# Kernel optimization log

Hardware: AMD Instinct MI355X
Metric: run time of the kernel (lower is better)

Reference implementation:

```python
import jax, jax.numpy as jnp
import numpy as np

S, H, I, E, K = 16384, 1024, 512, 64, 2
CAP = 640  # capacity per expert: ceil(S*K/E * 1.25)


def setup_inputs() -> dict:
    key = jax.random.key(0)
    k0, k1, k2, k3, k4 = jax.random.split(key, 5)
    x = jax.random.normal(k0, (S, H), jnp.float32)
    w_gate = jax.random.normal(k1, (H, E), jnp.float32) * 0.02
    wg = jax.random.normal(k2, (E, H, I), jnp.float32) * 0.02
    wu = jax.random.normal(k3, (E, H, I), jnp.float32) * 0.02
    wd = jax.random.normal(k4, (E, I, H), jnp.float32) * 0.02
    return {"x": x, "w_gate": w_gate, "wg": wg, "wu": wu, "wd": wd}


def reference(x, w_gate, wg, wu, wd):
    # --- gate (fp32) + softmax ---
    logits = x.astype(jnp.float32) @ w_gate                      # [S,E]
    prob = jax.nn.softmax(logits, axis=-1)
    topk_p, topk_e = jax.lax.top_k(prob, K)                      # [S,K]

    # --- capacity-based dispatch (token-major, route-minor order, as in torch loop) ---
    flat_e = topk_e.reshape(-1)                                  # [S*K]
    onehot = jax.nn.one_hot(flat_e, E, dtype=jnp.int32)          # [S*K,E]
    pos = jnp.cumsum(onehot, axis=0)[jnp.arange(S * K), flat_e] - 1  # slot within expert
    valid = pos < CAP                                            # [S*K]

    combine_w = jnp.where(valid.reshape(S, K), topk_p, 0.0)      # dropped -> 0 weight
    slot_idx = jnp.where(valid, flat_e * CAP + pos, E * CAP)     # dummy row for drops
    x_rep = jnp.repeat(x, K, axis=0)                             # [S*K,H], row i = x[i//K]
    y = jnp.zeros((E * CAP + 1, H), x.dtype).at[slot_idx].set(x_rep)[: E * CAP]
    dispatched = y.reshape(E, CAP, H)

    # --- per-expert SwiGLU MLP (grouped GEMMs) ---
    g = jnp.einsum("ech,ehi->eci", dispatched, wg)
    u = jnp.einsum("ech,ehi->eci", dispatched, wu)
    expert_out = jnp.einsum("eci,eih->ech", jax.nn.silu(g) * u, wd)  # [E,CAP,H]

    # --- normalize weights and combine (gather + weighted sum) ---
    cw = combine_w / jnp.clip(combine_w.sum(-1, keepdims=True), 1e-12, None)
    scatter_index = jnp.where(valid, flat_e * CAP + pos, -1).reshape(S, K)
    gathered = expert_out.reshape(E * CAP, H)[scatter_index]     # [S,K,H]; -1 wraps, weight=0
    out = jnp.einsum("sk,skh->sh", cw, gathered)                 # [S,H]

    router_loss = jnp.zeros((1,), jnp.float32)
    return out, cw, router_loss, logits
```

## Files before the change

### kernel.cpp

```cpp
#include <hip/hip_runtime.h>
#include <hip/hip_bf16.h>

constexpr int S_TOK = 16384;
constexpr int HDIM  = 1024;
constexpr int IDIM  = 512;
constexpr int NEXP  = 64;
constexpr int CAPC  = 640;
constexpr int NCHUNK = 128;

typedef __attribute__((ext_vector_type(8))) short bf16x8;
typedef __attribute__((ext_vector_type(4))) short short4v;
typedef __attribute__((ext_vector_type(4))) float f32x4;

__device__ __forceinline__ float bf2f(unsigned short u){
  return __uint_as_float(((unsigned)u) << 16);
}
__device__ __forceinline__ unsigned short f2bf(float f){
  unsigned u = __float_as_uint(f);
  return (unsigned short)((u + 0x7fffu + ((u >> 16) & 1u)) >> 16);
}
__device__ __forceinline__ unsigned pk2cvt(float a, float b){
  unsigned r;
  asm volatile("v_cvt_pk_bf16_f32 %0, %1, %2" : "=v"(r) : "v"(a), "v"(b));
  return r;
}
__device__ __forceinline__ void gload_lds16(const void* g, void* l){
  __builtin_amdgcn_global_load_lds((const __attribute__((address_space(1))) unsigned*)g,
                                   (__attribute__((address_space(3))) unsigned*)l, 16, 0, 0);
}
__device__ __forceinline__ unsigned ldsoff(const void* p){ return (unsigned)(size_t)p; }
__device__ __forceinline__ void trread2(unsigned addr, short4v& lo, short4v& hi){
  asm volatile("ds_read_b64_tr_b16 %0, %2\n\t"
               "ds_read_b64_tr_b16 %1, %2 offset:512"
               : "=&v"(lo), "=&v"(hi) : "v"(addr));
}

__global__ __launch_bounds__(256) void gate_kernel(
    const float* __restrict__ x, const float* __restrict__ wgate,
    float* __restrict__ logits_out, float* __restrict__ topk_p,
    int* __restrict__ flat_e, float* __restrict__ rl_out)
{
  __shared__ float xs[4][HDIM];
  const int w = threadIdx.x >> 6, lane = threadIdx.x & 63;
  const int tok = blockIdx.x * 4 + w;
  const float4* xr = (const float4*)(x + (size_t)tok * HDIM);
  float4* xd = (float4*)(&xs[w][0]);
#pragma unroll
  for (int j = 0; j < 4; ++j) xd[j * 64 + lane] = xr[j * 64 + lane];
  __syncthreads();
  float acc = 0.f;
#pragma unroll 8
  for (int h = 0; h < HDIM; ++h)
    acc = fmaf(xs[w][h], wgate[h * NEXP + lane], acc);
  logits_out[(size_t)tok * NEXP + lane] = acc;
  float m = acc;
#pragma unroll
  for (int d = 1; d < 64; d <<= 1) m = fmaxf(m, __shfl_xor(m, d));
  float p = expf(acc - m);
  float sum = p;
#pragma unroll
  for (int d = 1; d < 64; d <<= 1) sum += __shfl_xor(sum, d);
  float prob = p / sum;
  float v = prob; int idx = lane;
#pragma unroll
  for (int d = 1; d < 64; d <<= 1){
    float ov = __shfl_xor(v, d); int oi = __shfl_xor(idx, d);
    if (ov > v || (ov == v && oi < idx)){ v = ov; idx = oi; }
  }
  const int e1 = idx; const float p1 = v;
  v = (lane == e1) ? -1.f : prob; idx = lane;
#pragma unroll
  for (int d = 1; d < 64; d <<= 1){
    float ov = __shfl_xor(v, d); int oi = __shfl_xor(idx, d);
    if (ov > v || (ov == v && oi < idx)){ v = ov; idx = oi; }
  }
  if (lane == 0){
    flat_e[tok * 2]     = e1;  flat_e[tok * 2 + 1] = idx;
    topk_p[tok * 2]     = p1;  topk_p[tok * 2 + 1] = v;
  }
  if (tok == 0 && lane == 0) rl_out[0] = 0.f;
}

__global__ __launch_bounds__(256) void hist_kernel(const int* __restrict__ flat_e,
                                                   int* __restrict__ counts)
{
  __shared__ int hh[NEXP];
  const int t = threadIdx.x;
  if (t < NEXP) hh[t] = 0;
  __syncthreads();
  const int e = flat_e[blockIdx.x * 256 + t];
  atomicAdd(&hh[e], 1);
  __syncthreads();
  if (t < NEXP) counts[blockIdx.x * NEXP + t] = hh[t];
}

__global__ __launch_bounds__(256) void offsets_kernel(const int* __restrict__ counts,
                                                      int* __restrict__ offs,
                                                      int* __restrict__ etot)
{
  const int w = threadIdx.x >> 6, lane = threadIdx.x & 63;
  const int e = blockIdx.x * 4 + w;
  int v0 = counts[lane * NEXP + e];
  int v1 = counts[(64 + lane) * NEXP + e];
  int s0 = v0, s1 = v1;
#pragma unroll
  for (int d = 1; d < 64; d <<= 1){
    int n0 = __shfl_up(s0, d); if (lane >= d) s0 += n0;
    int n1 = __shfl_up(s1, d); if (lane >= d) s1 += n1;
  }
  const int tot0 = __shfl(s0, 63);
  offs[lane * NEXP + e]        = s0 - v0;
  offs[(64 + lane) * NEXP + e] = tot0 + s1 - v1;
  if (lane == 63) etot[e] = tot0 + s1;
}

__global__ __launch_bounds__(256) void place_kernel(
    const int* __restrict__ flat_e, const float* __restrict__ topk_p,
    const int* __restrict__ offs, int* __restrict__ entry_slot,
    int* __restrict__ token_of_slot, float* __restrict__ cw_out)
{
  __shared__ int es[256];
  __shared__ float wsh[256];
  const int t = threadIdx.x;
  const int i = blockIdx.x * 256 + t;
  const int e = flat_e[i];
  es[t] = e;
  __syncthreads();
  int local = 0;
  for (int j = 0; j < t; ++j) local += (es[j] == e);
  const int pos = offs[blockIdx.x * NEXP + e] + local;
  const bool valid = pos < CAPC;
  const int slot = e * CAPC + pos;
  entry_slot[i] = valid ? slot : -1;
  if (valid) token_of_slot[slot] = i >> 1;
  const float p = topk_p[i];
  wsh[t] = valid ? p : 0.f;
  __syncthreads();
  const float wme = wsh[t], wo = wsh[t ^ 1];
  cw_out[i] = wme / fmaxf(wme + wo, 1e-12f);
}

__global__ __launch_bounds__(256) void adisp_kernel(
    const float* __restrict__ x, const int* __restrict__ token_of_slot,
    const int* __restrict__ etot, unsigned short* __restrict__ adisp)
{
  const int slot = blockIdx.x;
  const int e = slot / CAPC, c = slot - e * CAPC;
  int cnt = etot[e]; if (cnt > CAPC) cnt = CAPC;
  if (c >= cnt) return;
  const int tok = token_of_slot[slot];
  const int t = threadIdx.x;
  float4 v = ((const float4*)(x + (size_t)tok * HDIM))[t];
  ushort4 o; o.x = f2bf(v.x); o.y = f2bf(v.y); o.z = f2bf(v.z); o.w = f2bf(v.w);
  ((ushort4*)(adisp + (size_t)slot * HDIM))[t] = o;
}


__global__ __launch_bounds__(512, 2) void gemm1_kernel(
    const unsigned short* __restrict__ adisp,
    const float* __restrict__ wg, const float* __restrict__ wu,
    const int* __restrict__ etot,
    unsigned short* __restrict__ hbuf)
{
  constexpr int NK1 = HDIM / 32;
  __shared__ unsigned short As[3][128 * 32];
  __shared__ unsigned short Bs[3][2 * 128 * 32];
  const int bb = blockIdx.x;
  const int lb = (bb & 7) * 160 + (bb >> 3);
  const int e = lb / 20; const int r2 = lb - e * 20;
  const int nt = r2 / 5, mt = r2 - nt * 5;
  { int cnt = etot[e]; if (cnt > CAPC) cnt = CAPC;
    if (mt * 128 >= cnt) return; }
  const int t = threadIdx.x, w = t >> 6, lane = t & 63;
  const int wr = w >> 2, wc = w & 3;
  const size_t arow0 = (size_t)e * CAPC + (size_t)mt * 128;
  const unsigned short* abase = adisp + arow0 * HDIM;
  const float* gsrc = wg + (size_t)e * HDIM * IDIM + nt * 128;
  const float* usrc = wu + (size_t)e * HDIM * IDIM + nt * 128;

  int aoff; { int row = t >> 2, jsrc = (t & 3) ^ ((row >> 1) & 3);
              aoff = row * HDIM + jsrc * 8; }
  const int g_ = w >> 1, par = w & 1;
  const int dk = (lane >> 1) & 3, h8 = lane & 1, ng = lane >> 3;
  const int bk = 8 * g_ + 4 * par + dk;
  const int bn0 = ng * 16 + h8 * 8;
  const int bgo = bk * IDIM + bn0;
  const unsigned bwo = (unsigned)((((ng * 2 + par) * 4 + g_) * 64) + dk * 16 + h8 * 8);

  f32x4 ag[4][2], au[4][2];
#pragma unroll
  for (int i = 0; i < 4; ++i)
#pragma unroll
    for (int j = 0; j < 2; ++j)
#pragma unroll
      for (int q = 0; q < 4; ++q){ ag[i][j][q] = 0.f; au[i][j][q] = 0.f; }

  float4 g0a, g0b, u0a, u0b, g1a, g1b, u1a, u1b;

#define G1_LOAD(KB, RA, RB, RC, RD) {                                          \
    const float* gp_ = gsrc + (size_t)(KB) * IDIM + bgo;                       \
    const float* up_ = usrc + (size_t)(KB) * IDIM + bgo;                       \
    RA = *(const float4*)gp_;       RB = *(const float4*)(gp_ + 4);            \
    RC = *(const float4*)up_;       RD = *(const float4*)(up_ + 4); }

#define G1_STORE(NB, WA, WB, WC, WD) {                                         \
    *(uint4*)&Bs[NB][bwo] = make_uint4(pk2cvt(WA.x,WA.y), pk2cvt(WA.z,WA.w),   \
                                       pk2cvt(WB.x,WB.y), pk2cvt(WB.z,WB.w));  \
    *(uint4*)&Bs[NB][4096 + bwo] = make_uint4(pk2cvt(WC.x,WC.y), pk2cvt(WC.z,WC.w), \
                                       pk2cvt(WD.x,WD.y), pk2cvt(WD.z,WD.w)); }

#define G1_STEP(TI, LA, LB, LC, LD, WA, WB, WC, WD) {                          \
    const int cur_ = (TI) % 3;                                                 \
    const bool pf_ = (TI) + 2 < NK1;                                           \
    if (pf_){                                                                  \
      const int kb2_ = ((TI) + 2) * 32;                                        \
      gload_lds16(abase + aoff + kb2_, &As[((TI) + 2) % 3][w * 64 * 8]);       \
      G1_LOAD(kb2_, LA, LB, LC, LD);                                           \
    }                                                                          \
    { const int j8_ = lane >> 4;                                               \
      bf16x8 af_[4], bg_[2], bu_[2];                                           \
      _Pragma("unroll")                                                        \
      for (int m = 0; m < 4; ++m){                                             \
        int row_ = wr * 64 + m * 16 + (lane & 15);                             \
        af_[m] = *(const bf16x8*)&As[cur_][row_ * 32 + ((j8_ ^ ((row_ >> 1) & 3)) * 8)]; \
      }                                                                        \
      const unsigned b0_ = ldsoff(&Bs[cur_][0]);                               \
      _Pragma("unroll")                                                        \
      for (int n = 0; n < 2; ++n){                                             \
        unsigned ao_ = (unsigned)((wc * 2 + n) * 1024 + lane * 8);             \
        short4v l0_, l1_, m0_, m1_;                                            \
        trread2(b0_ + ao_, l0_, l1_);                                          \
        bg_[n] = __builtin_shufflevector(l0_, l1_, 0,1,2,3,4,5,6,7);           \
        trread2(b0_ + 8192 + ao_, m0_, m1_);                                   \
        bu_[n] = __builtin_shufflevector(m0_, m1_, 0,1,2,3,4,5,6,7);           \
      }                                                                        \
      asm volatile("s_waitcnt lgkmcnt(0)" ::: "memory");                       \
      __builtin_amdgcn_sched_barrier(0);                                       \
      __builtin_amdgcn_s_setprio(1);                                           \
      _Pragma("unroll")                                                        \
      for (int m = 0; m < 4; ++m)                                              \
        _Pragma("unroll")                                                      \
        for (int n = 0; n < 2; ++n){                                           \
          ag[m][n] = __builtin_amdgcn_mfma_f32_16x16x32_bf16(af_[m], bg_[n], ag[m][n], 0, 0, 0); \
          au[m][n] = __builtin_amdgcn_mfma_f32_16x16x32_bf16(af_[m], bu_[n], au[m][n], 0, 0, 0); \
        }                                                                      \
      __builtin_amdgcn_s_setprio(0);                                           \
    }                                                                          \
    if ((TI) + 1 < NK1){                                                       \
      if (pf_) asm volatile("s_waitcnt vmcnt(5)" ::: "memory");                \
      else     asm volatile("s_waitcnt vmcnt(0)" ::: "memory");                \
      G1_STORE(((TI) + 1) % 3, WA, WB, WC, WD);                                \
    }                                                                          \
    asm volatile("s_waitcnt lgkmcnt(0)" ::: "memory");                         \
    __builtin_amdgcn_s_barrier();                                              \
    __builtin_amdgcn_sched_barrier(0);                                         \
  }

  gload_lds16(abase + aoff + 0,  &As[0][w * 64 * 8]);
  G1_LOAD(0,  g0a, g0b, u0a, u0b);
  gload_lds16(abase + aoff + 32, &As[1][w * 64 * 8]);
  G1_LOAD(32, g1a, g1b, u1a, u1b);
  asm volatile("s_waitcnt vmcnt(5)" ::: "memory");
  G1_STORE(0, g0a, g0b, u0a, u0b);
  asm volatile("s_waitcnt lgkmcnt(0)" ::: "memory");
  __builtin_amdgcn_s_barrier();

  for (int tb = 0; tb < NK1; tb += 2){
    G1_STEP(tb,     g0a, g0b, u0a, u0b,  g1a, g1b, u1a, u1b);
    G1_STEP(tb + 1, g1a, g1b, u1a, u1b,  g0a, g0b, u0a, u0b);
  }
#undef G1_STEP
#undef G1_STORE
#undef G1_LOAD

#pragma unroll
  for (int m = 0; m < 4; ++m)
#pragma unroll
    for (int n = 0; n < 2; ++n)
#pragma unroll
      for (int q = 0; q < 4; ++q){
        int row = wr * 64 + m * 16 + (lane >> 4) * 4 + q;
        int col = nt * 128 + wc * 32 + n * 16 + (lane & 15);
        float gv = ag[m][n][q], uv = au[m][n][q];
        float hv = gv / (1.f + expf(-gv)) * uv;
        hbuf[(arow0 + row) * IDIM + col] = f2bf(hv);
      }
}

__global__ __launch_bounds__(512, 2) void gemm2_kernel(
    const unsigned short* __restrict__ hbuf,
    const float* __restrict__ wd,
    const int* __restrict__ etot,
    unsigned short* __restrict__ eo)
{
  constexpr int NK2 = IDIM / 32;
  __shared__ unsigned short As[3][128 * 32];
  __shared__ unsigned short Bs[3][2 * 128 * 32];
  const int bb = blockIdx.x;
  const int lb = (bb & 7) * 160 + (bb >> 3);
  const int e = lb / 20; const int r2 = lb - e * 20;
  const int nt = r2 / 5, mt = r2 - nt * 5;
  { int cnt = etot[e]; if (cnt > CAPC) cnt = CAPC;
    if (mt * 128 >= cnt) return; }
  const int t = threadIdx.x, w = t >> 6, lane = t & 63;
  const int wr = w >> 2, wc = w & 3;
  const size_t arow0 = (size_t)e * CAPC + (size_t)mt * 128;
  const unsigned short* abase = hbuf + arow0 * IDIM;
  const float* dsrc = wd + (size_t)e * IDIM * HDIM + nt * 256;

  int aoff; { int row = t >> 2, jsrc = (t & 3) ^ ((row >> 1) & 3);
              aoff = row * IDIM + jsrc * 8; }
  const int g_ = w >> 1, par = w & 1;
  const int dk = (lane >> 1) & 3, h8 = lane & 1, ng = lane >> 3;
  const int bk = 8 * g_ + 4 * par + dk;
  const int bn0 = ng * 16 + h8 * 8;
  const int bgo = bk * HDIM + bn0;
  const unsigned bwo = (unsigned)((((ng * 2 + par) * 4 + g_) * 64) + dk * 16 + h8 * 8);

  f32x4 ac[4][4];
#pragma unroll
  for (int i = 0; i < 4; ++i)
#pragma unroll
    for (int j = 0; j < 4; ++j)
#pragma unroll
      for (int q = 0; q < 4; ++q) ac[i][j][q] = 0.f;

  float4 p0a, p0b, p1a, p1b, q0a, q0b, q1a, q1b;

#define G2_LOAD(KB, RA, RB, RC, RD) {                                          \
    const float* gp_ = dsrc + (size_t)(KB) * HDIM + bgo;                       \
    RA = *(const float4*)gp_;         RB = *(const float4*)(gp_ + 4);          \
    RC = *(const float4*)(gp_ + 128); RD = *(const float4*)(gp_ + 132); }

#define G2_STORE(NB, WA, WB, WC, WD) {                                         \
    *(uint4*)&Bs[NB][bwo] = make_uint4(pk2cvt(WA.x,WA.y), pk2cvt(WA.z,WA.w),   \
                                       pk2cvt(WB.x,WB.y), pk2cvt(WB.z,WB.w));  \
    *(uint4*)&Bs[NB][4096 + bwo] = make_uint4(pk2cvt(WC.x,WC.y), pk2cvt(WC.z,WC.w), \
                                       pk2cvt(WD.x,WD.y), pk2cvt(WD.z,WD.w)); }

#define G2_STEP(TI, LA, LB, LC, LD, WA, WB, WC, WD) {                          \
    const int cur_ = (TI) % 3;                                                 \
    const bool pf_ = (TI) + 2 < NK2;                                           \
    if (pf_){                                                                  \
      const int kb2_ = ((TI) + 2) * 32;                                        \
      gload_lds16(abase + aoff + kb2_, &As[((TI) + 2) % 3][w * 64 * 8]);       \
      G2_LOAD(kb2_, LA, LB, LC, LD);                                           \
    }                                                                          \
    { const int j8_ = lane >> 4;                                               \
      bf16x8 af_[4], bf_[4];                                                   \
      _Pragma("unroll")                                                        \
      for (int m = 0; m < 4; ++m){                                             \
        int row_ = wr * 64 + m * 16 + (lane & 15);                             \
        af_[m] = *(const bf16x8*)&As[cur_][row_ * 32 + ((j8_ ^ ((row_ >> 1) & 3)) * 8)]; \
      }                                                                        \
      const unsigned b0_ = ldsoff(&Bs[cur_][0]) + (unsigned)(wc >> 1) * 8192;  \
      _Pragma("unroll")                                                        \
      for (int n = 0; n < 4; ++n){                                             \
        unsigned ao_ = (unsigned)(((wc & 1) * 4 + n) * 1024 + lane * 8);       \
        short4v l0_, l1_;                                                      \
        trread2(b0_ + ao_, l0_, l1_);                                          \
        bf_[n] = __builtin_shufflevector(l0_, l1_, 0,1,2,3,4,5,6,7);           \
      }                                                                        \
      asm volatile("s_waitcnt lgkmcnt(0)" ::: "memory");                       \
      __builtin_amdgcn_sched_barrier(0);                                       \
      __builtin_amdgcn_s_setprio(1);                                           \
      _Pragma("unroll")                                                        \
      for (int m = 0; m < 4; ++m)                                              \
        _Pragma("unroll")                                                      \
        for (int n = 0; n < 4; ++n)                                            \
          ac[m][n] = __builtin_amdgcn_mfma_f32_16x16x32_bf16(af_[m], bf_[n], ac[m][n], 0, 0, 0); \
      __builtin_amdgcn_s_setprio(0);                                           \
    }                                                                          \
    if ((TI) + 1 < NK2){                                                       \
      if (pf_) asm volatile("s_waitcnt vmcnt(5)" ::: "memory");                \
      else     asm volatile("s_waitcnt vmcnt(0)" ::: "memory");                \
      G2_STORE(((TI) + 1) % 3, WA, WB, WC, WD);                                \
    }                                                                          \
    asm volatile("s_waitcnt lgkmcnt(0)" ::: "memory");                         \
    __builtin_amdgcn_s_barrier();                                              \
    __builtin_amdgcn_sched_barrier(0);                                         \
  }

  gload_lds16(abase + aoff + 0,  &As[0][w * 64 * 8]);
  G2_LOAD(0,  p0a, p0b, q0a, q0b);
  gload_lds16(abase + aoff + 32, &As[1][w * 64 * 8]);
  G2_LOAD(32, p1a, p1b, q1a, q1b);
  asm volatile("s_waitcnt vmcnt(5)" ::: "memory");
  G2_STORE(0, p0a, p0b, q0a, q0b);
  asm volatile("s_waitcnt lgkmcnt(0)" ::: "memory");
  __builtin_amdgcn_s_barrier();

  for (int tb = 0; tb < NK2; tb += 2){
    G2_STEP(tb,     p0a, p0b, q0a, q0b,  p1a, p1b, q1a, q1b);
    G2_STEP(tb + 1, p1a, p1b, q1a, q1b,  p0a, p0b, q0a, q0b);
  }
#undef G2_STEP
#undef G2_STORE
#undef G2_LOAD

#pragma unroll
  for (int m = 0; m < 4; ++m)
#pragma unroll
    for (int n = 0; n < 4; ++n)
#pragma unroll
      for (int q = 0; q < 4; ++q){
        int row = wr * 64 + m * 16 + (lane >> 4) * 4 + q;
        int col = nt * 256 + wc * 64 + n * 16 + (lane & 15);
        eo[(arow0 + row) * HDIM + col] = f2bf(ac[m][n][q]);
      }
}

__global__ __launch_bounds__(256) void combine_kernel(
    const unsigned short* __restrict__ eo, const int* __restrict__ entry_slot,
    const float* __restrict__ cw, float* __restrict__ out)
{
  const int s = blockIdx.x, t = threadIdx.x;
  const int s0 = entry_slot[2 * s], s1 = entry_slot[2 * s + 1];
  const float w0 = cw[2 * s], w1 = cw[2 * s + 1];
  const int c = t * 4;
  float r0 = 0.f, r1 = 0.f, r2 = 0.f, r3 = 0.f;
  if (s0 >= 0){
    ushort4 vq = *(const ushort4*)&eo[(size_t)s0 * HDIM + c];
    r0 += w0 * bf2f(vq.x); r1 += w0 * bf2f(vq.y); r2 += w0 * bf2f(vq.z); r3 += w0 * bf2f(vq.w);
  }
  if (s1 >= 0){
    ushort4 vq = *(const ushort4*)&eo[(size_t)s1 * HDIM + c];
    r0 += w1 * bf2f(vq.x); r1 += w1 * bf2f(vq.y); r2 += w1 * bf2f(vq.z); r3 += w1 * bf2f(vq.w);
  }
  ((float4*)(out + (size_t)s * HDIM))[t] = make_float4(r0, r1, r2, r3);
}

extern "C" void kernel_launch(void* const* d_in, const int* in_sizes, int n_in,
                              void* d_out, int out_size, void* d_ws, size_t ws_size,
                              hipStream_t stream) {
  (void)in_sizes; (void)n_in; (void)out_size; (void)ws_size;
  const float* x     = (const float*)d_in[0];
  const float* wgate = (const float*)d_in[1];
  const float* wg    = (const float*)d_in[2];
  const float* wu    = (const float*)d_in[3];
  const float* wd    = (const float*)d_in[4];

  float* out        = (float*)d_out;
  float* cw_out     = out + (size_t)S_TOK * HDIM;
  float* rl_out     = cw_out + (size_t)S_TOK * 2;
  float* logits_out = rl_out + 1;

  char* w8 = (char*)d_ws;
  size_t off = 0;
  auto alloc = [&](size_t bytes){ size_t r = off; off += (bytes + 255) & ~(size_t)255; return r; };
  int*   flat_e_ws        = (int*)  (w8 + alloc((size_t)32768 * 4));
  float* topk_p_ws        = (float*)(w8 + alloc((size_t)32768 * 4));
  int*   counts_ws        = (int*)  (w8 + alloc((size_t)NCHUNK * NEXP * 4));
  int*   offs_ws          = (int*)  (w8 + alloc((size_t)NCHUNK * NEXP * 4));
  int*   etot_ws          = (int*)  (w8 + alloc((size_t)NEXP * 4));
  int*   entry_slot_ws    = (int*)  (w8 + alloc((size_t)32768 * 4));
  int*   token_of_slot_ws = (int*)  (w8 + alloc((size_t)NEXP * CAPC * 4));
  unsigned short* hbuf_ws = (unsigned short*)(w8 + alloc((size_t)NEXP * CAPC * IDIM * 2));
  unsigned short* adisp_ws= (unsigned short*)(w8 + alloc((size_t)NEXP * CAPC * HDIM * 2));
  unsigned short* eo_ws   = adisp_ws;

  gate_kernel   <<<S_TOK / 4, 256, 0, stream>>>(x, wgate, logits_out, topk_p_ws, flat_e_ws, rl_out);
  hist_kernel   <<<NCHUNK,    256, 0, stream>>>(flat_e_ws, counts_ws);
  offsets_kernel<<<16,        256, 0, stream>>>(counts_ws, offs_ws, etot_ws);
  place_kernel  <<<NCHUNK,    256, 0, stream>>>(flat_e_ws, topk_p_ws, offs_ws,
                                                entry_slot_ws, token_of_slot_ws, cw_out);
  adisp_kernel  <<<NEXP * CAPC, 256, 0, stream>>>(x, token_of_slot_ws, etot_ws, adisp_ws);
  gemm1_kernel  <<<NEXP * 20, 512, 0, stream>>>(adisp_ws, wg, wu, etot_ws, hbuf_ws);
  gemm2_kernel  <<<NEXP * 20, 512, 0, stream>>>(hbuf_ws, wd, etot_ws, eo_ws);
  combine_kernel<<<S_TOK,     256, 0, stream>>>(eo_ws, entry_slot_ws, cw_out, out);
}
```

Baseline: 538.2 us.

## Switch grouped GEMMs to 32x32x16 MFMA with re-laid-out B tiles in LDS

Replaces the 16x16x32 bf16 MFMA tiling in both expert GEMM kernels with 32x32x16 MFMA instructions. The B-operand LDS layout, the transposed-read offsets and the epilogue row/column mapping are reworked to match the larger instruction shape. The aim is fewer MFMA and LDS read instructions per k-step and better operand reuse per instruction. The risks are different LDS bank-conflict patterns and accumulator register pressure from the 16-wide fragments.

```diff
diff --git a/kernel.cpp b/kernel.cpp
--- a/kernel.cpp
+++ b/kernel.cpp
@@ -10,7 +10,7 @@
 
 typedef __attribute__((ext_vector_type(8))) short bf16x8;
 typedef __attribute__((ext_vector_type(4))) short short4v;
-typedef __attribute__((ext_vector_type(4))) float f32x4;
+typedef __attribute__((ext_vector_type(16))) float f32x16;
 
 __device__ __forceinline__ float bf2f(unsigned short u){
   return __uint_as_float(((unsigned)u) << 16);
@@ -31,7 +31,7 @@
 __device__ __forceinline__ unsigned ldsoff(const void* p){ return (unsigned)(size_t)p; }
 __device__ __forceinline__ void trread2(unsigned addr, short4v& lo, short4v& hi){
   asm volatile("ds_read_b64_tr_b16 %0, %2\n\t"
-               "ds_read_b64_tr_b16 %1, %2 offset:512"
+               "ds_read_b64_tr_b16 %1, %2 offset:128"
                : "=&v"(lo), "=&v"(hi) : "v"(addr));
 }
 
@@ -180,20 +180,20 @@
 
   int aoff; { int row = t >> 2, jsrc = (t & 3) ^ ((row >> 1) & 3);
               aoff = row * HDIM + jsrc * 8; }
-  const int g_ = w >> 1, par = w & 1;
-  const int dk = (lane >> 1) & 3, h8 = lane & 1, ng = lane >> 3;
-  const int bk = 8 * g_ + 4 * par + dk;
-  const int bn0 = ng * 16 + h8 * 8;
+  const int ks_ = w >> 2, khalf = (w >> 1) & 1, par = w & 1;
+  const int dk = (lane >> 1) & 3, h8 = lane & 1;
+  const int n16 = (lane >> 3) & 1, n32 = lane >> 4;
+  const int bk = 16 * ks_ + 8 * khalf + 4 * par + dk;
+  const int bn0 = n32 * 32 + n16 * 16 + h8 * 8;
   const int bgo = bk * IDIM + bn0;
-  const unsigned bwo = (unsigned)((((ng * 2 + par) * 4 + g_) * 64) + dk * 16 + h8 * 8);
-
-  f32x4 ag[4][2], au[4][2];
-#pragma unroll
-  for (int i = 0; i < 4; ++i)
-#pragma unroll
-    for (int j = 0; j < 2; ++j)
-#pragma unroll
-      for (int q = 0; q < 4; ++q){ ag[i][j][q] = 0.f; au[i][j][q] = 0.f; }
+  const unsigned bwo = (unsigned)(n32 * 1024 + ks_ * 512 + (khalf * 2 + n16) * 128
+                                  + par * 64 + dk * 16 + h8 * 8);
+
+  f32x16 ag[2], au[2];
+#pragma unroll
+  for (int i = 0; i < 2; ++i)
+#pragma unroll
+    for (int q = 0; q < 16; ++q){ ag[i][q] = 0.f; au[i][q] = 0.f; }
 
   float4 g0a, g0b, u0a, u0b, g1a, g1b, u1a, u1b;
 
@@ -217,33 +217,28 @@
       gload_lds16(abase + aoff + kb2_, &As[((TI) + 2) % 3][w * 64 * 8]);       \
       G1_LOAD(kb2_, LA, LB, LC, LD);                                           \
     }                                                                          \
-    { const int j8_ = lane >> 4;                                               \
-      bf16x8 af_[4], bg_[2], bu_[2];                                           \
-      _Pragma("unroll")                                                        \
-      for (int m = 0; m < 4; ++m){                                             \
-        int row_ = wr * 64 + m * 16 + (lane & 15);                             \
-        af_[m] = *(const bf16x8*)&As[cur_][row_ * 32 + ((j8_ ^ ((row_ >> 1) & 3)) * 8)]; \
-      }                                                                        \
-      const unsigned b0_ = ldsoff(&Bs[cur_][0]);                               \
-      _Pragma("unroll")                                                        \
-      for (int n = 0; n < 2; ++n){                                             \
-        unsigned ao_ = (unsigned)((wc * 2 + n) * 1024 + lane * 8);             \
-        short4v l0_, l1_, m0_, m1_;                                            \
-        trread2(b0_ + ao_, l0_, l1_);                                          \
-        bg_[n] = __builtin_shufflevector(l0_, l1_, 0,1,2,3,4,5,6,7);           \
-        trread2(b0_ + 8192 + ao_, m0_, m1_);                                   \
-        bu_[n] = __builtin_shufflevector(m0_, m1_, 0,1,2,3,4,5,6,7);           \
-      }                                                                        \
+    const unsigned b0_ = ldsoff(&Bs[cur_][0]) + (unsigned)wc * 2048            \
+                         + (unsigned)(lane >> 4) * 256 + (unsigned)(lane & 15) * 8; \
+    _Pragma("unroll")                                                          \
+    for (int ksi = 0; ksi < 2; ++ksi){                                         \
+      bf16x8 af0_, af1_, bg_, bu_;                                             \
+      { int row0_ = wr * 64 + (lane & 31);                                     \
+        int row1_ = row0_ + 32;                                                \
+        int koct_ = ksi * 2 + (lane >> 5);                                     \
+        af0_ = *(const bf16x8*)&As[cur_][row0_ * 32 + ((koct_ ^ ((row0_ >> 1) & 3)) * 8)]; \
+        af1_ = *(const bf16x8*)&As[cur_][row1_ * 32 + ((koct_ ^ ((row1_ >> 1) & 3)) * 8)]; } \
+      { short4v l0_, l1_, m0_, m1_;                                            \
+        trread2(b0_ + (unsigned)ksi * 1024, l0_, l1_);                         \
+        bg_ = __builtin_shufflevector(l0_, l1_, 0,1,2,3,4,5,6,7);              \
+        trread2(b0_ + 8192 + (unsigned)ksi * 1024, m0_, m1_);                  \
+        bu_ = __builtin_shufflevector(m0_, m1_, 0,1,2,3,4,5,6,7); }            \
       asm volatile("s_waitcnt lgkmcnt(0)" ::: "memory");                       \
       __builtin_amdgcn_sched_barrier(0);                                       \
       __builtin_amdgcn_s_setprio(1);                                           \
-      _Pragma("unroll")                                                        \
-      for (int m = 0; m < 4; ++m)                                              \
-        _Pragma("unroll")                                                      \
-        for (int n = 0; n < 2; ++n){                                           \
-          ag[m][n] = __builtin_amdgcn_mfma_f32_16x16x32_bf16(af_[m], bg_[n], ag[m][n], 0, 0, 0); \
-          au[m][n] = __builtin_amdgcn_mfma_f32_16x16x32_bf16(af_[m], bu_[n], au[m][n], 0, 0, 0); \
-        }                                                                      \
+      ag[0] = __builtin_amdgcn_mfma_f32_32x32x16_bf16(af0_, bg_, ag[0], 0, 0, 0); \
+      au[0] = __builtin_amdgcn_mfma_f32_32x32x16_bf16(af0_, bu_, au[0], 0, 0, 0); \
+      ag[1] = __builtin_amdgcn_mfma_f32_32x32x16_bf16(af1_, bg_, ag[1], 0, 0, 0); \
+      au[1] = __builtin_amdgcn_mfma_f32_32x32x16_bf16(af1_, bu_, au[1], 0, 0, 0); \
       __builtin_amdgcn_s_setprio(0);                                           \
     }                                                                          \
     if ((TI) + 1 < NK1){                                                       \
@@ -274,17 +269,15 @@
 #undef G1_LOAD
 
 #pragma unroll
-  for (int m = 0; m < 4; ++m)
-#pragma unroll
-    for (int n = 0; n < 2; ++n)
-#pragma unroll
-      for (int q = 0; q < 4; ++q){
-        int row = wr * 64 + m * 16 + (lane >> 4) * 4 + q;
-        int col = nt * 128 + wc * 32 + n * 16 + (lane & 15);
-        float gv = ag[m][n][q], uv = au[m][n][q];
-        float hv = gv / (1.f + expf(-gv)) * uv;
-        hbuf[(arow0 + row) * IDIM + col] = f2bf(hv);
-      }
+  for (int mp = 0; mp < 2; ++mp)
+#pragma unroll
+    for (int r = 0; r < 16; ++r){
+      int row = wr * 64 + mp * 32 + (r & 3) + 8 * (r >> 2) + 4 * (lane >> 5);
+      int col = nt * 128 + wc * 32 + (lane & 31);
+      float gv = ag[mp][r], uv = au[mp][r];
+      float hv = gv / (1.f + expf(-gv)) * uv;
+      hbuf[(arow0 + row) * IDIM + col] = f2bf(hv);
+    }
 }
 
 __global__ __launch_bounds__(512, 2) void gemm2_kernel(
@@ -310,20 +303,22 @@
 
   int aoff; { int row = t >> 2, jsrc = (t & 3) ^ ((row >> 1) & 3);
               aoff = row * IDIM + jsrc * 8; }
-  const int g_ = w >> 1, par = w & 1;
-  const int dk = (lane >> 1) & 3, h8 = lane & 1, ng = lane >> 3;
-  const int bk = 8 * g_ + 4 * par + dk;
-  const int bn0 = ng * 16 + h8 * 8;
+  const int ks_ = w >> 2, khalf = (w >> 1) & 1, par = w & 1;
+  const int dk = (lane >> 1) & 3, h8 = lane & 1;
+  const int n16 = (lane >> 3) & 1, n32 = lane >> 4;
+  const int bk = 16 * ks_ + 8 * khalf + 4 * par + dk;
+  const int bn0 = n32 * 32 + n16 * 16 + h8 * 8;
   const int bgo = bk * HDIM + bn0;
-  const unsigned bwo = (unsigned)((((ng * 2 + par) * 4 + g_) * 64) + dk * 16 + h8 * 8);
-
-  f32x4 ac[4][4];
-#pragma unroll
-  for (int i = 0; i < 4; ++i)
-#pragma unroll
-    for (int j = 0; j < 4; ++j)
-#pragma unroll
-      for (int q = 0; q < 4; ++q) ac[i][j][q] = 0.f;
+  const unsigned bwo = (unsigned)(n32 * 1024 + ks_ * 512 + (khalf * 2 + n16) * 128
+                                  + par * 64 + dk * 16 + h8 * 8);
+
+  f32x16 ac[2][2];
+#pragma unroll
+  for (int i = 0; i < 2; ++i)
+#pragma unroll
+    for (int j = 0; j < 2; ++j)
+#pragma unroll
+      for (int q = 0; q < 16; ++q) ac[i][j][q] = 0.f;
 
   float4 p0a, p0b, p1a, p1b, q0a, q0b, q1a, q1b;
 
@@ -346,29 +341,28 @@
       gload_lds16(abase + aoff + kb2_, &As[((TI) + 2) % 3][w * 64 * 8]);       \
       G2_LOAD(kb2_, LA, LB, LC, LD);                                           \
     }                                                                          \
-    { const int j8_ = lane >> 4;                                               \
-      bf16x8 af_[4], bf_[4];                                                   \
-      _Pragma("unroll")                                                        \
-      for (int m = 0; m < 4; ++m){                                             \
-        int row_ = wr * 64 + m * 16 + (lane & 15);                             \
-        af_[m] = *(const bf16x8*)&As[cur_][row_ * 32 + ((j8_ ^ ((row_ >> 1) & 3)) * 8)]; \
-      }                                                                        \
-      const unsigned b0_ = ldsoff(&Bs[cur_][0]) + (unsigned)(wc >> 1) * 8192;  \
-      _Pragma("unroll")                                                        \
-      for (int n = 0; n < 4; ++n){                                             \
-        unsigned ao_ = (unsigned)(((wc & 1) * 4 + n) * 1024 + lane * 8);       \
-        short4v l0_, l1_;                                                      \
-        trread2(b0_ + ao_, l0_, l1_);                                          \
-        bf_[n] = __builtin_shufflevector(l0_, l1_, 0,1,2,3,4,5,6,7);           \
-      }                                                                        \
+    const unsigned b0_ = ldsoff(&Bs[cur_][0]) + (unsigned)wc * 4096            \
+                         + (unsigned)(lane >> 4) * 256 + (unsigned)(lane & 15) * 8; \
+    _Pragma("unroll")                                                          \
+    for (int ksi = 0; ksi < 2; ++ksi){                                         \
+      bf16x8 af0_, af1_, b0f_, b1f_;                                           \
+      { int row0_ = wr * 64 + (lane & 31);                                     \
+        int row1_ = row0_ + 32;                                                \
+        int koct_ = ksi * 2 + (lane >> 5);                                     \
+        af0_ = *(const bf16x8*)&As[cur_][row0_ * 32 + ((koct_ ^ ((row0_ >> 1) & 3)) * 8)]; \
+        af1_ = *(const bf16x8*)&As[cur_][row1_ * 32 + ((koct_ ^ ((row1_ >> 1) & 3)) * 8)]; } \
+      { short4v l0_, l1_, m0_, m1_;                                            \
+        trread2(b0_ + (unsigned)ksi * 1024, l0_, l1_);                         \
+        b0f_ = __builtin_shufflevector(l0_, l1_, 0,1,2,3,4,5,6,7);             \
+        trread2(b0_ + 2048 + (unsigned)ksi * 1024, m0_, m1_);                  \
+        b1f_ = __builtin_shufflevector(m0_, m1_, 0,1,2,3,4,5,6,7); }           \
       asm volatile("s_waitcnt lgkmcnt(0)" ::: "memory");                       \
       __builtin_amdgcn_sched_barrier(0);                                       \
       __builtin_amdgcn_s_setprio(1);                                           \
-      _Pragma("unroll")                                                        \
-      for (int m = 0; m < 4; ++m)                                              \
-        _Pragma("unroll")                                                      \
-        for (int n = 0; n < 4; ++n)                                            \
-          ac[m][n] = __builtin_amdgcn_mfma_f32_16x16x32_bf16(af_[m], bf_[n], ac[m][n], 0, 0, 0); \
+      ac[0][0] = __builtin_amdgcn_mfma_f32_32x32x16_bf16(af0_, b0f_, ac[0][0], 0, 0, 0); \
+      ac[0][1] = __builtin_amdgcn_mfma_f32_32x32x16_bf16(af0_, b1f_, ac[0][1], 0, 0, 0); \
+      ac[1][0] = __builtin_amdgcn_mfma_f32_32x32x16_bf16(af1_, b0f_, ac[1][0], 0, 0, 0); \
+      ac[1][1] = __builtin_amdgcn_mfma_f32_32x32x16_bf16(af1_, b1f_, ac[1][1], 0, 0, 0); \
       __builtin_amdgcn_s_setprio(0);                                           \
     }                                                                          \
     if ((TI) + 1 < NK2){                                                       \
@@ -399,14 +393,14 @@
 #undef G2_LOAD
 
 #pragma unroll
-  for (int m = 0; m < 4; ++m)
-#pragma unroll
-    for (int n = 0; n < 4; ++n)
-#pragma unroll
-      for (int q = 0; q < 4; ++q){
-        int row = wr * 64 + m * 16 + (lane >> 4) * 4 + q;
-        int col = nt * 256 + wc * 64 + n * 16 + (lane & 15);
-        eo[(arow0 + row) * HDIM + col] = f2bf(ac[m][n][q]);
+  for (int mp = 0; mp < 2; ++mp)
+#pragma unroll
+    for (int np = 0; np < 2; ++np)
+#pragma unroll
+      for (int r = 0; r < 16; ++r){
+        int row = wr * 64 + mp * 32 + (r & 3) + 8 * (r >> 2) + 4 * (lane >> 5);
+        int col = nt * 256 + wc * 64 + np * 32 + (lane & 31);
+        eo[(arow0 + row) * HDIM + col] = f2bf(ac[mp][np][r]);
       }
 }
 
```

New measurement: 514.4 us. 1.05x faster.
